# Kernel optimization log

Measured on AMD Instinct MI355X. Metric: run time of the kernel, lower is better.

The kernel has to match this reference:

```python
import jax, jax.numpy as jnp
import numpy as np

N_NODES = 20000
STEPS = 10  # message_passing_steps


def _mlp(x, p):
    # 3-layer MLP: Linear->ReLU->Linear->ReLU->Linear (no final activation)
    W1, b1, W2, b2, W3, b3 = p
    h = jax.nn.relu(x @ W1 + b1)
    h = jax.nn.relu(h @ W2 + b2)
    return h @ W3 + b3


def _aggregate(dst, edge_attr, num_nodes):
    # scatter_add of edge features into destination nodes, degree-normalized (deg clamped to >=1)
    agg = jax.ops.segment_sum(edge_attr, dst, num_segments=num_nodes)
    deg = jax.ops.segment_sum(jnp.ones((dst.shape[0], 1), edge_attr.dtype), dst, num_segments=num_nodes)
    return agg / jnp.maximum(deg, 1.0)


def setup_inputs() -> dict:
    key = jax.random.key(0)
    N, EM, EC = N_NODES, 120000, 20000
    ND, MD, CD, OD, L = 12, 7, 4, 3, 128
    keys = iter(jax.random.split(key, 128))

    def lin(i, o):
        return (jax.random.normal(next(keys), (i, o), jnp.float32) * 0.05,
                jax.random.normal(next(keys), (o,), jnp.float32) * 0.05)

    inp = {
        "node_x": jax.random.normal(next(keys), (N, ND), jnp.float32),
        "mesh_edge_attr": jax.random.normal(next(keys), (EM, MD), jnp.float32),
        "contact_edge_attr": jax.random.normal(next(keys), (EC, CD), jnp.float32),
    }
    dims = {"ne": (ND, L), "me": (MD, L), "ce": (CD, L), "pe": (3 * L, L), "pn": (3 * L, L), "de": (L, OD)}
    for name, (i, o) in dims.items():
        W1, b1 = lin(i, L)
        W2, b2 = lin(L, L)
        W3, b3 = lin(L, o)
        for pn, p in zip(["W1", "b1", "W2", "b2", "W3", "b3"], [W1, b1, W2, b2, W3, b3]):
            inp[name + "_" + pn] = p
    inp["mesh_edge_index"] = jax.random.randint(next(keys), (2, EM), 0, N)
    inp["contact_edge_index"] = jax.random.randint(next(keys), (2, EC), 0, N)
    return inp


def reference(node_x, mesh_edge_attr, contact_edge_attr,
              ne_W1, ne_b1, ne_W2, ne_b2, ne_W3, ne_b3,
              me_W1, me_b1, me_W2, me_b2, me_W3, me_b3,
              ce_W1, ce_b1, ce_W2, ce_b2, ce_W3, ce_b3,
              pe_W1, pe_b1, pe_W2, pe_b2, pe_W3, pe_b3,
              pn_W1, pn_b1, pn_W2, pn_b2, pn_W3, pn_b3,
              de_W1, de_b1, de_W2, de_b2, de_W3, de_b3,
              mesh_edge_index, contact_edge_index):
    ne = (ne_W1, ne_b1, ne_W2, ne_b2, ne_W3, ne_b3)
    mep = (me_W1, me_b1, me_W2, me_b2, me_W3, me_b3)
    cep = (ce_W1, ce_b1, ce_W2, ce_b2, ce_W3, ce_b3)
    pe = (pe_W1, pe_b1, pe_W2, pe_b2, pe_W3, pe_b3)
    pn = (pn_W1, pn_b1, pn_W2, pn_b2, pn_W3, pn_b3)
    de = (de_W1, de_b1, de_W2, de_b2, de_W3, de_b3)
    N = node_x.shape[0]
    # encode
    x = _mlp(node_x, ne)                 # [N, 128]
    me = _mlp(mesh_edge_attr, mep)       # [EM, 128]
    ce = _mlp(contact_edge_attr, cep)    # [EC, 128]
    msrc, mdst = mesh_edge_index[0], mesh_edge_index[1]
    csrc, cdst = contact_edge_index[0], contact_edge_index[1]
    # process (shared edge_mlp for both edge types, residual updates)
    for _ in range(STEPS):
        me = me + _mlp(jnp.concatenate([x[msrc], x[mdst], me], axis=-1), pe)
        ce = ce + _mlp(jnp.concatenate([x[csrc], x[cdst], ce], axis=-1), pe)
        agg_m = _aggregate(mdst, me, N)
        agg_c = _aggregate(cdst, ce, N)
        x = x + _mlp(jnp.concatenate([x, agg_m, agg_c], axis=-1), pn)
    # decode
    return _mlp(x, de)                   # [N, 3]
```

## Files before the change

kernel.cpp:

```cpp
#include <hip/hip_runtime.h>
#include <stdint.h>

typedef unsigned short u16;
typedef __attribute__((ext_vector_type(8))) short bf16x8;
typedef __attribute__((ext_vector_type(4))) float f32x4;

#define NNODES 20000
#define EM 120000
#define EC 20000
#define LDIM 128
#define MT 32
#define MT2 64
#define A_STR 392
#define H_STR 136
#define D_STR 132

__device__ __forceinline__ u16 f2bf(float f){
  uint32_t b = __float_as_uint(f);
  b += 0x7FFF + ((b >> 16) & 1);
  return (u16)(b >> 16);
}

__device__ __forceinline__ f32x4 mfma16(bf16x8 a, bf16x8 b, f32x4 c){
  return __builtin_amdgcn_mfma_f32_16x16x32_bf16(a, b, c, 0, 0, 0);
}

template<int KB>
__device__ __forceinline__ void layer(const u16* sIn, int in_str, const u16* Wp,
                                      int wr, int wc, int lane, f32x4 acc[4]){
  const int row = wr*16 + (lane & 15);
  const int kg  = lane >> 4;
  #pragma unroll
  for (int kb = 0; kb < KB; ++kb){
    bf16x8 a = *(const bf16x8*)(sIn + row*in_str + kb*32 + kg*8);
    const u16* wb = Wp + (((kb*8 + wc*4)*64 + lane) << 3);
    #pragma unroll
    for (int nf = 0; nf < 4; ++nf){
      bf16x8 b = *(const bf16x8*)(wb + (nf << 9));
      acc[nf] = mfma16(a, b, acc[nf]);
    }
  }
}

__device__ __forceinline__ void hid_epi(f32x4 acc[4], const float* bias,
                                        int wr, int wc, int lane, u16* sOut){
  const int cl = lane & 15;
  const int r0 = wr*16 + (lane >> 4)*4;
  #pragma unroll
  for (int nf = 0; nf < 4; ++nf){
    int col = wc*64 + nf*16 + cl;
    float bv = bias[col];
    #pragma unroll
    for (int r = 0; r < 4; ++r){
      float v = acc[nf][r] + bv;
      sOut[(r0 + r)*H_STR + col] = f2bf(v > 0.f ? v : 0.f);
    }
  }
}

__device__ __forceinline__ void zero4(f32x4 acc[4]){
  const f32x4 vz = {0.f, 0.f, 0.f, 0.f};
  #pragma unroll
  for (int i = 0; i < 4; ++i) acc[i] = vz;
}

template<int KB, int STR>
__device__ __forceinline__ void layer64(const u16* sIn, const u16* Wp,
                                        int wr, int wc, int lane, f32x4 acc[2][2]){
  const int r0 = wr*32 + (lane & 15);
  const int kg = lane >> 4;
  const u16* a0p = sIn + r0*STR + kg*8;
  const u16* a1p = a0p + 16*STR;
  const u16* wb  = Wp + (((wc*2)*64 + lane) << 3);
  #pragma unroll
  for (int kb = 0; kb < KB; ++kb){
    bf16x8 a0 = *(const bf16x8*)(a0p + kb*32);
    bf16x8 a1 = *(const bf16x8*)(a1p + kb*32);
    const u16* wk = wb + kb*4096;
    bf16x8 b0 = *(const bf16x8*)(wk);
    bf16x8 b1 = *(const bf16x8*)(wk + 512);
    acc[0][0] = mfma16(a0, b0, acc[0][0]);
    acc[1][0] = mfma16(a1, b0, acc[1][0]);
    acc[0][1] = mfma16(a0, b1, acc[0][1]);
    acc[1][1] = mfma16(a1, b1, acc[1][1]);
  }
}

template<int STR>
__device__ __forceinline__ void hid_epi64(f32x4 acc[2][2], const float* bias,
                                          int wr, int wc, int lane, u16* sOut){
  const int cl = lane & 15;
  const int rq = (lane >> 4)*4;
  #pragma unroll
  for (int rf = 0; rf < 2; ++rf){
    int r0 = wr*32 + rf*16 + rq;
    #pragma unroll
    for (int nf = 0; nf < 2; ++nf){
      int col = wc*32 + nf*16 + cl;
      float bv = bias[col];
      #pragma unroll
      for (int r = 0; r < 4; ++r){
        float v = acc[rf][nf][r] + bv;
        sOut[(r0 + r)*STR + col] = f2bf(v > 0.f ? v : 0.f);
      }
    }
  }
}

__device__ __forceinline__ void zero22(f32x4 acc[2][2]){
  const f32x4 vz = {0.f, 0.f, 0.f, 0.f};
  acc[0][0] = vz; acc[0][1] = vz; acc[1][0] = vz; acc[1][1] = vz;
}

template<int KB, int STR>
__device__ __forceinline__ void layer32(const u16* sIn, const u16* Wp,
                                        int wr, int wc, int lane, f32x4 acc[2]){
  const int r0 = wr*16 + (lane & 15);
  const int kg = lane >> 4;
  const u16* a0p = sIn + r0*STR + kg*8;
  const u16* wb  = Wp + (((wc*2)*64 + lane) << 3);
  #pragma unroll
  for (int kb = 0; kb < KB; ++kb){
    bf16x8 a0 = *(const bf16x8*)(a0p + kb*32);
    const u16* wk = wb + kb*4096;
    bf16x8 b0 = *(const bf16x8*)(wk);
    bf16x8 b1 = *(const bf16x8*)(wk + 512);
    acc[0] = mfma16(a0, b0, acc[0]);
    acc[1] = mfma16(a0, b1, acc[1]);
  }
}

template<int STR>
__device__ __forceinline__ void hid_epi32(f32x4 acc[2], const float* bias,
                                          int wr, int wc, int lane, u16* sOut){
  const int cl = lane & 15;
  const int r0 = wr*16 + (lane >> 4)*4;
  #pragma unroll
  for (int nf = 0; nf < 2; ++nf){
    int col = wc*32 + nf*16 + cl;
    float bv = bias[col];
    #pragma unroll
    for (int r = 0; r < 4; ++r){
      float v = acc[nf][r] + bv;
      sOut[(r0 + r)*STR + col] = f2bf(v > 0.f ? v : 0.f);
    }
  }
}

struct PackDesc { const float* src; int K_raw, N_raw, NF, elem_off; };
struct PackArgs { PackDesc d[18]; int total; };

__global__ __launch_bounds__(256) void pack_weights(PackArgs pa, u16* dst){
  int idx = blockIdx.x*256 + threadIdx.x;
  if (idx >= pa.total) return;
  int di = 0;
  #pragma unroll
  for (int i = 1; i < 18; ++i) if (idx >= pa.d[i].elem_off) di = i;
  PackDesc dd = pa.d[di];
  int e = idx - dd.elem_off;
  int f = e >> 9, lane = (e >> 3) & 63, j = e & 7;
  int kb = f / dd.NF, nf = f % dd.NF;
  int k = kb*32 + (lane >> 4)*8 + j;
  int n = nf*16 + (lane & 15);
  float v = (k < dd.K_raw && n < dd.N_raw) ? dd.src[k*dd.N_raw + n] : 0.f;
  dst[idx] = f2bf(v);
}

__global__ __launch_bounds__(256) void hist_kernel(const int* mdst, const int* cdst,
                                                   int* cnt_m, int* cnt_c){
  int i = blockIdx.x*256 + threadIdx.x;
  if (i < EM) atomicAdd(&cnt_m[mdst[i]], 1);
  else if (i < EM + EC) atomicAdd(&cnt_c[cdst[i - EM]], 1);
}

struct ScanArgs { const int *cnt_m, *cnt_c; int *start_m, *start_c, *cur_m, *cur_c; };

__global__ __launch_bounds__(256) void scan_kernel(ScanArgs a){
  const int n = NNODES;
  const int* cnt = blockIdx.x == 0 ? a.cnt_m : a.cnt_c;
  int* start     = blockIdx.x == 0 ? a.start_m : a.start_c;
  int* cur       = blockIdx.x == 0 ? a.cur_m : a.cur_c;
  __shared__ int part[256];
  __shared__ int base[257];
  int t = threadIdx.x;
  const int per = (n + 255) / 256;
  int lo = t*per, hi = min(n, lo + per);
  int s = 0;
  for (int j = lo; j < hi; ++j) s += cnt[j];
  part[t] = s;
  __syncthreads();
  if (t == 0){
    int run = 0;
    for (int i = 0; i < 256; ++i){ base[i] = run; run += part[i]; }
    base[256] = run;
  }
  __syncthreads();
  int run = base[t];
  for (int j = lo; j < hi; ++j){ start[j] = run; cur[j] = run; run += cnt[j]; }
  if (t == 255) start[n] = base[256];
}

__global__ __launch_bounds__(256) void scatter_kernel(const int* mdst, const int* cdst,
                                                      int* cur_m, int* cur_c,
                                                      int* eid_m, int* eid_c){
  int i = blockIdx.x*256 + threadIdx.x;
  if (i < EM){
    int p = atomicAdd(&cur_m[mdst[i]], 1);
    eid_m[p] = i;
  } else if (i < EM + EC){
    int e = i - EM;
    int p = atomicAdd(&cur_c[cdst[e]], 1);
    eid_c[p] = e;
  }
}

struct EncArgs {
  const float* in; int Kraw;
  const u16 *Wp1, *Wp2, *Wp3;
  const float *b1, *b2, *b3;
  float* out_f32; u16* out_b16;
};

__global__ __launch_bounds__(256) void enc_kernel(EncArgs a){
  __shared__ u16 sA[MT*A_STR];
  __shared__ u16 sH[MT*H_STR];
  const int tid = threadIdx.x, lane = tid & 63, w = tid >> 6, wr = w & 1, wc = w >> 1;
  const int m0 = blockIdx.x * MT;
  for (int i = tid; i < MT*32; i += 256){
    int row = i >> 5, c = i & 31;
    float v = (c < a.Kraw) ? a.in[(size_t)(m0 + row)*a.Kraw + c] : 0.f;
    sA[row*A_STR + c] = f2bf(v);
  }
  __syncthreads();
  f32x4 acc[4]; zero4(acc);
  layer<1>(sA, A_STR, a.Wp1, wr, wc, lane, acc);
  hid_epi(acc, a.b1, wr, wc, lane, sH);
  __syncthreads();
  zero4(acc);
  layer<4>(sH, H_STR, a.Wp2, wr, wc, lane, acc);
  hid_epi(acc, a.b2, wr, wc, lane, sA);
  __syncthreads();
  zero4(acc);
  layer<4>(sA, H_STR, a.Wp3, wr, wc, lane, acc);
  const int cl = lane & 15, r0l = wr*16 + (lane >> 4)*4;
  #pragma unroll
  for (int nf = 0; nf < 4; ++nf){
    int col = wc*64 + nf*16 + cl;
    float bv = a.b3[col];
    #pragma unroll
    for (int r = 0; r < 4; ++r){
      int m = m0 + r0l + r;
      float v = acc[nf][r] + bv;
      a.out_f32[(size_t)m*LDIM + col] = v;
      if (a.out_b16) a.out_b16[(size_t)m*LDIM + col] = f2bf(v);
    }
  }
}

struct EdgeArgs {
  const u16 *Wp1, *Wp2, *Wp3;
  const float *b1, *b2, *b3;
  const u16* x_b16;
  const int *msrc, *mdst, *csrc, *cdst;
  float *me_f32, *ce_f32;
  int mesh_blocks;
};

__global__ __launch_bounds__(512, 6) void edge_kernel(EdgeArgs a){
  __shared__ u16 sCat[MT2*A_STR];
  const int tid = threadIdx.x, lane = tid & 63, w = tid >> 6, wr = w & 1, wc = w >> 1;
  const bool mesh = (int)blockIdx.x < a.mesh_blocks;
  const int e0 = (mesh ? (int)blockIdx.x : (int)blockIdx.x - a.mesh_blocks) * MT2;
  const int E = mesh ? EM : EC;
  const int* src = mesh ? a.msrc : a.csrc;
  const int* dst = mesh ? a.mdst : a.cdst;
  float* ff = mesh ? a.me_f32 : a.ce_f32;

  #pragma unroll
  for (int i = tid; i < MT2*32; i += 512){
    int row = i >> 5, c = i & 31;
    int e = e0 + row; if (e >= E) e = E - 1;
    const u16* sp = (c < 16) ? a.x_b16 + (size_t)src[e]*LDIM + c*8
                             : a.x_b16 + (size_t)dst[e]*LDIM + (c-16)*8;
    *(bf16x8*)(sCat + row*A_STR + c*8) = *(const bf16x8*)sp;
  }
  const int srow = tid >> 3, sj = tid & 7;
  int se = e0 + srow; if (se >= E) se = E - 1;
  const f32x4* fp = (const f32x4*)(ff + (size_t)se*LDIM + sj*16);
  f32x4 p0 = fp[0], p1 = fp[1], p2 = fp[2], p3 = fp[3];
  {
    bf16x8 t0, t1;
    #pragma unroll
    for (int k = 0; k < 4; ++k){
      t0[k] = (short)f2bf(p0[k]); t0[k+4] = (short)f2bf(p1[k]);
      t1[k] = (short)f2bf(p2[k]); t1[k+4] = (short)f2bf(p3[k]);
    }
    *(bf16x8*)(sCat + srow*A_STR + 256 + sj*16) = t0;
    *(bf16x8*)(sCat + srow*A_STR + 256 + sj*16 + 8) = t1;
  }
  __syncthreads();

  f32x4 acc[2][2]; zero22(acc);
  layer64<12, A_STR>(sCat, a.Wp1, wr, wc, lane, acc);
  __syncthreads();
  hid_epi64<A_STR>(acc, a.b1, wr, wc, lane, sCat + 256);
  __syncthreads();
  zero22(acc);
  layer64<4, A_STR>(sCat + 256, a.Wp2, wr, wc, lane, acc);
  hid_epi64<A_STR>(acc, a.b2, wr, wc, lane, sCat);
  __syncthreads();
  zero22(acc);
  layer64<4, A_STR>(sCat, a.Wp3, wr, wc, lane, acc);
  __syncthreads();

  float* dd = (float*)sCat;
  {
    const int cl = lane & 15, rq = (lane >> 4)*4;
    #pragma unroll
    for (int rf = 0; rf < 2; ++rf){
      #pragma unroll
      for (int nf = 0; nf < 2; ++nf){
        int col = wc*32 + nf*16 + cl;
        float bv = a.b3[col];
        #pragma unroll
        for (int r = 0; r < 4; ++r)
          dd[(wr*32 + rf*16 + rq + r)*D_STR + col] = acc[rf][nf][r] + bv;
      }
    }
  }
  __syncthreads();
  if (e0 + srow < E){
    float* op = ff + (size_t)(e0 + srow)*LDIM + sj*16;
    const f32x4* dp = (const f32x4*)(dd + srow*D_STR + sj*16);
    f32x4 n0 = p0 + dp[0], n1 = p1 + dp[1], n2 = p2 + dp[2], n3 = p3 + dp[3];
    ((f32x4*)op)[0] = n0; ((f32x4*)op)[1] = n1; ((f32x4*)op)[2] = n2; ((f32x4*)op)[3] = n3;
  }
}

struct NodeArgs {
  const u16 *Wp1, *Wp2, *Wp3;
  const float *b1, *b2, *b3;
  const u16* x_b16_in;
  const float *me_f32, *ce_f32;
  const int *start_m, *eid_m, *start_c, *eid_c;
  float* x_f32; u16* x_b16_out;
};

__global__ __launch_bounds__(512, 6) void node_kernel(NodeArgs a){
  __shared__ u16 sA[MT*A_STR];
  const int tid = threadIdx.x, lane = tid & 63, w = tid >> 6, wr = w & 1, wc = w >> 1;
  const int n0 = blockIdx.x * MT;

  {
    int row = tid >> 4, ch = tid & 15;
    *(bf16x8*)(sA + row*A_STR + ch*8) =
        *(const bf16x8*)(a.x_b16_in + (size_t)(n0+row)*LDIM + ch*8);
  }
  {
    const int r = tid >> 4, c0 = (tid & 15) * 8;
    const int n = n0 + r;
    {
      int s = a.start_m[n], e = a.start_m[n+1];
      f32x4 a0{0,0,0,0}, a1{0,0,0,0};
      for (int j = s; j < e; ++j){
        const f32x4* p = (const f32x4*)(a.me_f32 + (size_t)a.eid_m[j]*LDIM + c0);
        a0 += p[0]; a1 += p[1];
      }
      float inv = 1.f / fmaxf((float)(e - s), 1.f);
      bf16x8 t;
      #pragma unroll
      for (int k = 0; k < 4; ++k){ t[k] = (short)f2bf(a0[k]*inv); t[k+4] = (short)f2bf(a1[k]*inv); }
      *(bf16x8*)(sA + r*A_STR + 128 + c0) = t;
    }
    {
      int s = a.start_c[n], e = a.start_c[n+1];
      f32x4 a0{0,0,0,0}, a1{0,0,0,0};
      for (int j = s; j < e; ++j){
        const f32x4* p = (const f32x4*)(a.ce_f32 + (size_t)a.eid_c[j]*LDIM + c0);
        a0 += p[0]; a1 += p[1];
      }
      float inv = 1.f / fmaxf((float)(e - s), 1.f);
      bf16x8 t;
      #pragma unroll
      for (int k = 0; k < 4; ++k){ t[k] = (short)f2bf(a0[k]*inv); t[k+4] = (short)f2bf(a1[k]*inv); }
      *(bf16x8*)(sA + r*A_STR + 256 + c0) = t;
    }
  }
  __syncthreads();

  f32x4 acc[2]; acc[0] = f32x4{0,0,0,0}; acc[1] = f32x4{0,0,0,0};
  layer32<12, A_STR>(sA, a.Wp1, wr, wc, lane, acc);
  __syncthreads();
  hid_epi32<A_STR>(acc, a.b1, wr, wc, lane, sA + 256);
  __syncthreads();
  acc[0] = f32x4{0,0,0,0}; acc[1] = f32x4{0,0,0,0};
  layer32<4, A_STR>(sA + 256, a.Wp2, wr, wc, lane, acc);
  hid_epi32<A_STR>(acc, a.b2, wr, wc, lane, sA);
  __syncthreads();
  acc[0] = f32x4{0,0,0,0}; acc[1] = f32x4{0,0,0,0};
  layer32<4, A_STR>(sA, a.Wp3, wr, wc, lane, acc);

  const int cl = lane & 15, rq = (lane >> 4)*4;
  #pragma unroll
  for (int r = 0; r < 4; ++r){
    int n = n0 + wr*16 + rq + r;
    #pragma unroll
    for (int nf = 0; nf < 2; ++nf){
      int col = wc*32 + nf*16 + cl;
      float nv = a.x_f32[(size_t)n*LDIM + col] + acc[nf][r] + a.b3[col];
      a.x_f32[(size_t)n*LDIM + col] = nv;
      a.x_b16_out[(size_t)n*LDIM + col] = f2bf(nv);
    }
  }
}

struct DecArgs {
  const u16 *Wp1, *Wp2, *Wp3;
  const float *b1, *b2, *b3;
  const u16* x_b16; float* out;
};

__global__ __launch_bounds__(256) void dec_kernel(DecArgs a){
  __shared__ u16 sA[MT*A_STR];
  __shared__ u16 sH[MT*H_STR];
  const int tid = threadIdx.x, lane = tid & 63, w = tid >> 6, wr = w & 1, wc = w >> 1;
  const int n0 = blockIdx.x * MT;
  for (int i = tid; i < MT*16; i += 256){
    int row = i >> 4, ch = i & 15;
    *(bf16x8*)(sA + row*H_STR + ch*8) = *(const bf16x8*)(a.x_b16 + (size_t)(n0+row)*LDIM + ch*8);
  }
  __syncthreads();
  f32x4 acc[4]; zero4(acc);
  layer<4>(sA, H_STR, a.Wp1, wr, wc, lane, acc);
  hid_epi(acc, a.b1, wr, wc, lane, sH);
  __syncthreads();
  zero4(acc);
  layer<4>(sH, H_STR, a.Wp2, wr, wc, lane, acc);
  hid_epi(acc, a.b2, wr, wc, lane, sA);
  __syncthreads();
  if (wc == 0){
    f32x4 a3 = {0.f, 0.f, 0.f, 0.f};
    const int row = wr*16 + (lane & 15), kg = lane >> 4;
    #pragma unroll
    for (int kb = 0; kb < 4; ++kb){
      bf16x8 av = *(const bf16x8*)(sA + row*H_STR + kb*32 + kg*8);
      bf16x8 bv = *(const bf16x8*)(a.Wp3 + ((kb*64 + lane) << 3));
      a3 = mfma16(av, bv, a3);
    }
    const int cl = lane & 15, r0l = wr*16 + (lane >> 4)*4;
    if (cl < 3){
      #pragma unroll
      for (int r = 0; r < 4; ++r)
        a.out[(size_t)(n0 + r0l + r)*3 + cl] = a3[r] + a.b3[cl];
    }
  }
}

extern "C" void kernel_launch(void* const* d_in, const int* in_sizes, int n_in,
                              void* d_out, int out_size, void* d_ws, size_t ws_size,
                              hipStream_t stream){
  auto F = [&](int i){ return (const float*)d_in[i]; };
  const float* node_x   = F(0);
  const float* mesh_attr = F(1);
  const float* cont_attr = F(2);
  const int* mei = (const int*)d_in[39];
  const int* cei = (const int*)d_in[40];
  const int *msrc = mei, *mdst = mei + EM, *csrc = cei, *cdst = cei + EC;

  char* ws = (char*)d_ws;
  size_t off = 0;
  auto take = [&](size_t b)->void*{ void* p = ws + off; off += (b + 255) & ~(size_t)255; return p; };
  float* x_f32  = (float*)take((size_t)NNODES*LDIM*4);
  u16*   x_b16  = (u16*)  take((size_t)NNODES*LDIM*2);
  float* me_f32 = (float*)take((size_t)EM*LDIM*4);
  float* ce_f32 = (float*)take((size_t)EC*LDIM*4);
  u16*   wpack  = (u16*)  take((size_t)309248*2);
  int* cnt_m   = (int*)take((size_t)NNODES*4);
  int* cnt_c   = (int*)take((size_t)NNODES*4);
  int* start_m = (int*)take((size_t)(NNODES+1)*4);
  int* start_c = (int*)take((size_t)(NNODES+1)*4);
  int* cur_m   = (int*)take((size_t)NNODES*4);
  int* cur_c   = (int*)take((size_t)NNODES*4);
  int* eid_m   = (int*)take((size_t)EM*4);
  int* eid_c   = (int*)take((size_t)EC*4);

  static const int tbl[18][5] = {
    {3,12,128,32,128},{5,128,128,128,128},{7,128,128,128,128},
    {9,7,128,32,128},{11,128,128,128,128},{13,128,128,128,128},
    {15,4,128,32,128},{17,128,128,128,128},{19,128,128,128,128},
    {21,384,128,384,128},{23,128,128,128,128},{25,128,128,128,128},
    {27,384,128,384,128},{29,128,128,128,128},{31,128,128,128,128},
    {33,128,128,128,128},{35,128,128,128,128},{37,128,3,128,16}};
  PackArgs pa; int eo = 0; int offs[18];
  for (int i = 0; i < 18; ++i){
    offs[i] = eo;
    pa.d[i].src = F(tbl[i][0]);
    pa.d[i].K_raw = tbl[i][1];
    pa.d[i].N_raw = tbl[i][2];
    pa.d[i].NF = tbl[i][4] / 16;
    pa.d[i].elem_off = eo;
    eo += tbl[i][3] * tbl[i][4];
  }
  pa.total = eo;
  pack_weights<<<dim3(eo/256), dim3(256), 0, stream>>>(pa, wpack);

  size_t cnt_span = ((char*)cnt_c - (char*)cnt_m) + (size_t)NNODES*4;
  hipMemsetAsync(cnt_m, 0, cnt_span, stream);
  hist_kernel<<<dim3((EM + EC + 255)/256), dim3(256), 0, stream>>>(mdst, cdst, cnt_m, cnt_c);
  ScanArgs sa{cnt_m, cnt_c, start_m, start_c, cur_m, cur_c};
  scan_kernel<<<dim3(2), dim3(256), 0, stream>>>(sa);
  scatter_kernel<<<dim3((EM + EC + 255)/256), dim3(256), 0, stream>>>(mdst, cdst, cur_m, cur_c, eid_m, eid_c);

  EncArgs en{node_x, 12, wpack+offs[0], wpack+offs[1], wpack+offs[2], F(4), F(6), F(8), x_f32, x_b16};
  enc_kernel<<<dim3(NNODES/MT), dim3(256), 0, stream>>>(en);
  EncArgs em{mesh_attr, 7, wpack+offs[3], wpack+offs[4], wpack+offs[5], F(10), F(12), F(14), me_f32, nullptr};
  enc_kernel<<<dim3(EM/MT), dim3(256), 0, stream>>>(em);
  EncArgs ec{cont_attr, 4, wpack+offs[6], wpack+offs[7], wpack+offs[8], F(16), F(18), F(20), ce_f32, nullptr};
  enc_kernel<<<dim3(EC/MT), dim3(256), 0, stream>>>(ec);

  EdgeArgs ea;
  ea.Wp1 = wpack+offs[9]; ea.Wp2 = wpack+offs[10]; ea.Wp3 = wpack+offs[11];
  ea.b1 = F(22); ea.b2 = F(24); ea.b3 = F(26);
  ea.x_b16 = x_b16;
  ea.msrc = msrc; ea.mdst = mdst; ea.csrc = csrc; ea.cdst = cdst;
  ea.me_f32 = me_f32; ea.ce_f32 = ce_f32;
  ea.mesh_blocks = EM/MT2;

  NodeArgs na;
  na.Wp1 = wpack+offs[12]; na.Wp2 = wpack+offs[13]; na.Wp3 = wpack+offs[14];
  na.b1 = F(28); na.b2 = F(30); na.b3 = F(32);
  na.x_b16_in = x_b16;
  na.me_f32 = me_f32; na.ce_f32 = ce_f32;
  na.start_m = start_m; na.eid_m = eid_m; na.start_c = start_c; na.eid_c = eid_c;
  na.x_f32 = x_f32; na.x_b16_out = x_b16;

  const int edge_blocks = EM/MT2 + (EC + MT2 - 1)/MT2;
  const int node_blocks = NNODES/MT;
  for (int s = 0; s < 10; ++s){
    edge_kernel<<<dim3(edge_blocks), dim3(512), 0, stream>>>(ea);
    node_kernel<<<dim3(node_blocks), dim3(512), 0, stream>>>(na);
  }

  DecArgs da{wpack+offs[15], wpack+offs[16], wpack+offs[17], F(34), F(36), F(38), x_b16, (float*)d_out};
  dec_kernel<<<dim3(NNODES/MT), dim3(256), 0, stream>>>(da);
}
```

Measured before the change: 1.165 ms.

## Store edge features in destination-sorted order to make aggregation contiguous

```diff
diff --git a/kernel.cpp b/kernel.cpp
--- a/kernel.cpp
+++ b/kernel.cpp
@@ -202,15 +202,29 @@
 
 __global__ __launch_bounds__(256) void scatter_kernel(const int* mdst, const int* cdst,
                                                       int* cur_m, int* cur_c,
-                                                      int* eid_m, int* eid_c){
+                                                      int* pos_m, int* pos_c){
   int i = blockIdx.x*256 + threadIdx.x;
   if (i < EM){
     int p = atomicAdd(&cur_m[mdst[i]], 1);
-    eid_m[p] = i;
+    pos_m[i] = p;
   } else if (i < EM + EC){
     int e = i - EM;
     int p = atomicAdd(&cur_c[cdst[e]], 1);
-    eid_c[p] = e;
+    pos_c[e] = p;
+  }
+}
+
+__global__ __launch_bounds__(256) void permsd_kernel(const int* msrc, const int* mdst, const int* pos_m,
+                                                     const int* csrc, const int* cdst, const int* pos_c,
+                                                     int* sp_m, int* dp_m, int* sp_c, int* dp_c){
+  int i = blockIdx.x*256 + threadIdx.x;
+  if (i < EM){
+    int p = pos_m[i];
+    sp_m[p] = msrc[i]; dp_m[p] = mdst[i];
+  } else if (i < EM + EC){
+    int e = i - EM;
+    int p = pos_c[e];
+    sp_c[p] = csrc[e]; dp_c[p] = cdst[e];
   }
 }
 
@@ -219,6 +233,7 @@
   const u16 *Wp1, *Wp2, *Wp3;
   const float *b1, *b2, *b3;
   float* out_f32; u16* out_b16;
+  const int* perm;
 };
 
 __global__ __launch_bounds__(256) void enc_kernel(EncArgs a){
@@ -250,9 +265,10 @@
     #pragma unroll
     for (int r = 0; r < 4; ++r){
       int m = m0 + r0l + r;
+      int om = a.perm ? a.perm[m] : m;
       float v = acc[nf][r] + bv;
-      a.out_f32[(size_t)m*LDIM + col] = v;
-      if (a.out_b16) a.out_b16[(size_t)m*LDIM + col] = f2bf(v);
+      a.out_f32[(size_t)om*LDIM + col] = v;
+      if (a.out_b16) a.out_b16[(size_t)om*LDIM + col] = f2bf(v);
     }
   }
 }
@@ -261,7 +277,7 @@
   const u16 *Wp1, *Wp2, *Wp3;
   const float *b1, *b2, *b3;
   const u16* x_b16;
-  const int *msrc, *mdst, *csrc, *cdst;
+  const int *sp_m, *dp_m, *sp_c, *dp_c;
   float *me_f32, *ce_f32;
   int mesh_blocks;
 };
@@ -272,17 +288,17 @@
   const bool mesh = (int)blockIdx.x < a.mesh_blocks;
   const int e0 = (mesh ? (int)blockIdx.x : (int)blockIdx.x - a.mesh_blocks) * MT2;
   const int E = mesh ? EM : EC;
-  const int* src = mesh ? a.msrc : a.csrc;
-  const int* dst = mesh ? a.mdst : a.cdst;
+  const int* sp = mesh ? a.sp_m : a.sp_c;
+  const int* dp = mesh ? a.dp_m : a.dp_c;
   float* ff = mesh ? a.me_f32 : a.ce_f32;
 
   #pragma unroll
   for (int i = tid; i < MT2*32; i += 512){
     int row = i >> 5, c = i & 31;
     int e = e0 + row; if (e >= E) e = E - 1;
-    const u16* sp = (c < 16) ? a.x_b16 + (size_t)src[e]*LDIM + c*8
-                             : a.x_b16 + (size_t)dst[e]*LDIM + (c-16)*8;
-    *(bf16x8*)(sCat + row*A_STR + c*8) = *(const bf16x8*)sp;
+    const u16* xp = (c < 16) ? a.x_b16 + (size_t)sp[e]*LDIM + c*8
+                             : a.x_b16 + (size_t)dp[e]*LDIM + (c-16)*8;
+    *(bf16x8*)(sCat + row*A_STR + c*8) = *(const bf16x8*)xp;
   }
   const int srow = tid >> 3, sj = tid & 7;
   int se = e0 + srow; if (se >= E) se = E - 1;
@@ -331,8 +347,8 @@
   __syncthreads();
   if (e0 + srow < E){
     float* op = ff + (size_t)(e0 + srow)*LDIM + sj*16;
-    const f32x4* dp = (const f32x4*)(dd + srow*D_STR + sj*16);
-    f32x4 n0 = p0 + dp[0], n1 = p1 + dp[1], n2 = p2 + dp[2], n3 = p3 + dp[3];
+    const f32x4* dp_ = (const f32x4*)(dd + srow*D_STR + sj*16);
+    f32x4 n0 = p0 + dp_[0], n1 = p1 + dp_[1], n2 = p2 + dp_[2], n3 = p3 + dp_[3];
     ((f32x4*)op)[0] = n0; ((f32x4*)op)[1] = n1; ((f32x4*)op)[2] = n2; ((f32x4*)op)[3] = n3;
   }
 }
@@ -342,7 +358,7 @@
   const float *b1, *b2, *b3;
   const u16* x_b16_in;
   const float *me_f32, *ce_f32;
-  const int *start_m, *eid_m, *start_c, *eid_c;
+  const int *start_m, *start_c;
   float* x_f32; u16* x_b16_out;
 };
 
@@ -363,7 +379,7 @@
       int s = a.start_m[n], e = a.start_m[n+1];
       f32x4 a0{0,0,0,0}, a1{0,0,0,0};
       for (int j = s; j < e; ++j){
-        const f32x4* p = (const f32x4*)(a.me_f32 + (size_t)a.eid_m[j]*LDIM + c0);
+        const f32x4* p = (const f32x4*)(a.me_f32 + (size_t)j*LDIM + c0);
         a0 += p[0]; a1 += p[1];
       }
       float inv = 1.f / fmaxf((float)(e - s), 1.f);
@@ -376,7 +392,7 @@
       int s = a.start_c[n], e = a.start_c[n+1];
       f32x4 a0{0,0,0,0}, a1{0,0,0,0};
       for (int j = s; j < e; ++j){
-        const f32x4* p = (const f32x4*)(a.ce_f32 + (size_t)a.eid_c[j]*LDIM + c0);
+        const f32x4* p = (const f32x4*)(a.ce_f32 + (size_t)j*LDIM + c0);
         a0 += p[0]; a1 += p[1];
       }
       float inv = 1.f / fmaxf((float)(e - s), 1.f);
@@ -481,8 +497,12 @@
   int* start_c = (int*)take((size_t)(NNODES+1)*4);
   int* cur_m   = (int*)take((size_t)NNODES*4);
   int* cur_c   = (int*)take((size_t)NNODES*4);
-  int* eid_m   = (int*)take((size_t)EM*4);
-  int* eid_c   = (int*)take((size_t)EC*4);
+  int* pos_m   = (int*)take((size_t)EM*4);
+  int* pos_c   = (int*)take((size_t)EC*4);
+  int* sp_m    = (int*)take((size_t)EM*4);
+  int* dp_m    = (int*)take((size_t)EM*4);
+  int* sp_c    = (int*)take((size_t)EC*4);
+  int* dp_c    = (int*)take((size_t)EC*4);
 
   static const int tbl[18][5] = {
     {3,12,128,32,128},{5,128,128,128,128},{7,128,128,128,128},
@@ -509,20 +529,22 @@
   hist_kernel<<<dim3((EM + EC + 255)/256), dim3(256), 0, stream>>>(mdst, cdst, cnt_m, cnt_c);
   ScanArgs sa{cnt_m, cnt_c, start_m, start_c, cur_m, cur_c};
   scan_kernel<<<dim3(2), dim3(256), 0, stream>>>(sa);
-  scatter_kernel<<<dim3((EM + EC + 255)/256), dim3(256), 0, stream>>>(mdst, cdst, cur_m, cur_c, eid_m, eid_c);
-
-  EncArgs en{node_x, 12, wpack+offs[0], wpack+offs[1], wpack+offs[2], F(4), F(6), F(8), x_f32, x_b16};
+  scatter_kernel<<<dim3((EM + EC + 255)/256), dim3(256), 0, stream>>>(mdst, cdst, cur_m, cur_c, pos_m, pos_c);
+  permsd_kernel<<<dim3((EM + EC + 255)/256), dim3(256), 0, stream>>>(msrc, mdst, pos_m, csrc, cdst, pos_c,
+                                                                     sp_m, dp_m, sp_c, dp_c);
+
+  EncArgs en{node_x, 12, wpack+offs[0], wpack+offs[1], wpack+offs[2], F(4), F(6), F(8), x_f32, x_b16, nullptr};
   enc_kernel<<<dim3(NNODES/MT), dim3(256), 0, stream>>>(en);
-  EncArgs em{mesh_attr, 7, wpack+offs[3], wpack+offs[4], wpack+offs[5], F(10), F(12), F(14), me_f32, nullptr};
+  EncArgs em{mesh_attr, 7, wpack+offs[3], wpack+offs[4], wpack+offs[5], F(10), F(12), F(14), me_f32, nullptr, pos_m};
   enc_kernel<<<dim3(EM/MT), dim3(256), 0, stream>>>(em);
-  EncArgs ec{cont_attr, 4, wpack+offs[6], wpack+offs[7], wpack+offs[8], F(16), F(18), F(20), ce_f32, nullptr};
+  EncArgs ec{cont_attr, 4, wpack+offs[6], wpack+offs[7], wpack+offs[8], F(16), F(18), F(20), ce_f32, nullptr, pos_c};
   enc_kernel<<<dim3(EC/MT), dim3(256), 0, stream>>>(ec);
 
   EdgeArgs ea;
   ea.Wp1 = wpack+offs[9]; ea.Wp2 = wpack+offs[10]; ea.Wp3 = wpack+offs[11];
   ea.b1 = F(22); ea.b2 = F(24); ea.b3 = F(26);
   ea.x_b16 = x_b16;
-  ea.msrc = msrc; ea.mdst = mdst; ea.csrc = csrc; ea.cdst = cdst;
+  ea.sp_m = sp_m; ea.dp_m = dp_m; ea.sp_c = sp_c; ea.dp_c = dp_c;
   ea.me_f32 = me_f32; ea.ce_f32 = ce_f32;
   ea.mesh_blocks = EM/MT2;
 
@@ -531,7 +553,7 @@
   na.b1 = F(28); na.b2 = F(30); na.b3 = F(32);
   na.x_b16_in = x_b16;
   na.me_f32 = me_f32; na.ce_f32 = ce_f32;
-  na.start_m = start_m; na.eid_m = eid_m; na.start_c = start_c; na.eid_c = eid_c;
+  na.start_m = start_m; na.start_c = start_c;
   na.x_f32 = x_f32; na.x_b16_out = x_b16;
 
   const int edge_blocks = EM/MT2 + (EC + MT2 - 1)/MT2;
```

New measurement: 1.150 ms. About the same (-1.2%).
